# Performance work log

Measured on AMD Instinct MI355X. Metric: run time of the kernel, lower is better.

Reference implementation:

```python
import jax, jax.numpy as jnp
import numpy as np

B, N, D = 8, 2048, 256      # batch, tokens, model dim (= out_token_dims)
S = 128                     # query_key_dims
H = int(2.0 * D)            # expansion_factor * D = 512
EPS = 1e-5


def setup_inputs() -> dict:
    key = jax.random.key(0)
    ks = jax.random.split(key, 4)
    x = jax.random.normal(ks[0], (B, N, D), dtype=jnp.float32)
    g = jnp.ones((), jnp.float32)                                # ScaleNorm gain
    W_uv = jax.random.normal(ks[1], (D, 2 * H + S), jnp.float32) * 0.02
    b_uv = jnp.zeros((2 * H + S,), jnp.float32)
    gamma = jnp.ones((2, S), jnp.float32)                        # OffsetScale scale
    beta = jnp.zeros((2, S), jnp.float32)                        # OffsetScale offset
    W_o = jax.random.normal(ks[2], (H, D), jnp.float32) * 0.02
    b_o = jnp.zeros((D,), jnp.float32)
    return {"x": x, "g": g, "W_uv": W_uv, "b_uv": b_uv,
            "gamma": gamma, "beta": beta, "W_o": W_o, "b_o": b_o}


def reference(x, g, W_uv, b_uv, gamma, beta, W_o, b_o):
    d = x.shape[-1]
    # ScaleNorm: x / max(||x|| / sqrt(d), eps) * g
    norm = jnp.linalg.norm(x, axis=-1, keepdims=True) * jax.lax.rsqrt(jnp.float32(d))
    xn = x / jnp.maximum(norm, EPS) * g
    # fused uv projection + SiLU
    uv = jax.nn.silu(jnp.einsum('bnd,de->bne', xn, W_uv) + b_uv)
    u = uv[..., :H]            # gate branch        [B,N,H]
    v = uv[..., H:2 * H]       # value branch       [B,N,H]
    base = uv[..., 2 * H:]     # shared q/k base    [B,N,S]
    # OffsetScale heads=2 -> q, k (cheap per-dim affine)
    q = base * gamma[0] + beta[0]
    k = base * gamma[1] + beta[1]
    # single-head scores + ReLU^2 attention activation
    qk = jnp.einsum('bns,bms->bnm', q, k) * jax.lax.rsqrt(jnp.float32(S))
    attn = jnp.square(jax.nn.relu(qk))
    # gate * (attn @ v), then output projection back to D
    gated = u * jnp.einsum('bnm,bmh->bnh', attn, v)
    return jnp.einsum('bnh,hd->bnd', gated, W_o) + b_o
```

## Files before the change

kernel.cpp:

```cpp
#include <hip/hip_runtime.h>
#include <math.h>

#define BB 8
#define NN 2048
#define DD 256
#define SS 128
#define HH 512
#define EE 1152

typedef short bf16x8 __attribute__((ext_vector_type(8)));
typedef float f32x4 __attribute__((ext_vector_type(4)));

__device__ __forceinline__ short f2bf(float f) {
    union { float f; unsigned u; } a; a.f = f;
    unsigned r = a.u + 0x7FFFu + ((a.u >> 16) & 1u);
    return (short)(r >> 16);
}
__device__ __forceinline__ float bf2f(short s) {
    union { unsigned u; float f; } a; a.u = ((unsigned)(unsigned short)s) << 16;
    return a.f;
}
__device__ __forceinline__ void gl_lds16(const short* g, short* l) {
    __builtin_amdgcn_global_load_lds(
        (const __attribute__((address_space(1))) void*)g,
        (__attribute__((address_space(3))) void*)l, 16, 0, 0);
}

__global__ __launch_bounds__(256) void k_pre(
        const float* __restrict__ x, const float* __restrict__ gp,
        short* __restrict__ xn,
        const float* __restrict__ Wuv, const float* __restrict__ Wo,
        short* __restrict__ Wuv_t, short* __restrict__ Wo_t) {
    __shared__ float tile[32][33];
    int bid = blockIdx.x;
    int t = threadIdx.x;
    if (bid < 4096) {
        int wave = t >> 6, lane = t & 63;
        long row = (long)bid * 4 + wave;
        float4 xv = ((const float4*)(x + row * DD))[lane];
        float ss = xv.x*xv.x + xv.y*xv.y + xv.z*xv.z + xv.w*xv.w;
        #pragma unroll
        for (int off = 32; off > 0; off >>= 1) ss += __shfl_down(ss, off);
        ss = __shfl(ss, 0);
        float norm = sqrtf(ss) * 0.0625f;
        float scale = gp[0] / fmaxf(norm, 1e-5f);
        short4 o;
        o.x = f2bf(xv.x * scale); o.y = f2bf(xv.y * scale);
        o.z = f2bf(xv.z * scale); o.w = f2bf(xv.w * scale);
        ((short4*)(xn + row * DD))[lane] = o;
    } else if (bid < 4384) {
        int bid2 = bid - 4096;
        int et = bid2 % 36, dt = bid2 / 36;
        #pragma unroll
        for (int i = 0; i < 4; i++) {
            int idx = t + i*256, r = idx >> 5, c = idx & 31;
            tile[r][c] = Wuv[(long)(dt*32 + r)*EE + et*32 + c];
        }
        __syncthreads();
        #pragma unroll
        for (int i = 0; i < 4; i++) {
            int idx = t + i*256, r = idx >> 5, c = idx & 31;
            Wuv_t[(long)(et*32 + r)*DD + dt*32 + c] = f2bf(tile[c][r]);
        }
    } else {
        int bid3 = bid - 4384;
        int ht = bid3 % 16, dt = bid3 / 16;
        #pragma unroll
        for (int i = 0; i < 4; i++) {
            int idx = t + i*256, r = idx >> 5, c = idx & 31;
            tile[r][c] = Wo[(long)(ht*32 + r)*DD + dt*32 + c];
        }
        __syncthreads();
        #pragma unroll
        for (int i = 0; i < 4; i++) {
            int idx = t + i*256, r = idx >> 5, c = idx & 31;
            Wo_t[(long)(dt*32 + r)*HH + ht*32 + c] = f2bf(tile[c][r]);
        }
    }
}

__global__ __launch_bounds__(256) void k_gemm1(
        const short* __restrict__ xn, const short* __restrict__ Wuv_t,
        const float* __restrict__ b_uv,
        const float* __restrict__ gamma, const float* __restrict__ beta,
        short* __restrict__ u, short* __restrict__ vfrag,
        short* __restrict__ q, short* __restrict__ k) {
    __shared__ short As[128*64];
    __shared__ short Bs[128*64];
    int m0 = blockIdx.x * 128, n0 = blockIdx.y * 128;
    int t = threadIdx.x, w = t >> 6, lane = t & 63;
    int wr = w & 1, wc = w >> 1, l16 = lane & 15, quad = lane >> 4;
    int lr = lane >> 3, lc = (lane & 7) * 8;
    f32x4 acc[4][4] = {};
    for (int k0 = 0; k0 < DD; k0 += 64) {
        __syncthreads();
        #pragma unroll
        for (int i = 0; i < 4; i++) {
            int r0 = i*32 + w*8;
            gl_lds16(&xn[(long)(m0 + r0 + lr)*DD + k0 + lc], &As[r0*64]);
            gl_lds16(&Wuv_t[(long)(n0 + r0 + lr)*DD + k0 + lc], &Bs[r0*64]);
        }
        __syncthreads();
        #pragma unroll
        for (int kk = 0; kk < 2; kk++) {
            bf16x8 a[4], bb[4];
            #pragma unroll
            for (int mt = 0; mt < 4; mt++)
                a[mt] = *(const bf16x8*)&As[(wr*64 + mt*16 + l16)*64 + kk*32 + quad*8];
            #pragma unroll
            for (int nt = 0; nt < 4; nt++)
                bb[nt] = *(const bf16x8*)&Bs[(wc*64 + nt*16 + l16)*64 + kk*32 + quad*8];
            #pragma unroll
            for (int mt = 0; mt < 4; mt++)
                #pragma unroll
                for (int nt = 0; nt < 4; nt++)
                    acc[mt][nt] = __builtin_amdgcn_mfma_f32_16x16x32_bf16(
                        a[mt], bb[nt], acc[mt][nt], 0,0,0);
        }
    }
    #pragma unroll
    for (int mt = 0; mt < 4; mt++)
    #pragma unroll
    for (int nt = 0; nt < 4; nt++) {
        int gm0 = m0 + wr*64 + mt*16 + quad*4;
        int ge  = n0 + wc*64 + nt*16 + l16;
        float val[4];
        #pragma unroll
        for (int r = 0; r < 4; r++) {
            float xv = acc[mt][nt][r] + b_uv[ge];
            val[r] = xv / (1.0f + __expf(-xv));
        }
        if (ge < HH) {
            #pragma unroll
            for (int r = 0; r < 4; r++)
                u[(long)(gm0 + r)*HH + ge] = f2bf(val[r]);
        } else if (ge < 2*HH) {
            int h = ge - HH;
            long base = (((long)((gm0 >> 11)*64 + ((gm0 & 2047) >> 5)) * 32)
                         + (h >> 4)) * 512
                        + ((((gm0 & 31) >> 3)*16 + (h & 15)) * 8) + (gm0 & 7);
            short4 o;
            o.x = f2bf(val[0]); o.y = f2bf(val[1]);
            o.z = f2bf(val[2]); o.w = f2bf(val[3]);
            *(short4*)&vfrag[base] = o;
        } else {
            int si = ge - 2*HH;
            #pragma unroll
            for (int r = 0; r < 4; r++) {
                q[(long)(gm0 + r)*SS + si] = f2bf(val[r] * gamma[si]      + beta[si]);
                k[(long)(gm0 + r)*SS + si] = f2bf(val[r] * gamma[SS + si] + beta[SS + si]);
            }
        }
    }
}

#define KS(p,row)  (smem + ((p)*32 + (row))*136)
#define PS(p,row)  (smem + 8704 + ((p)*64 + (row))*40)
#define GT(hf,row) (smem + (hf)*16896 + (row)*264)

__global__ __launch_bounds__(512, 2) void k_attn(
        const short* __restrict__ q, const short* __restrict__ k,
        const short* __restrict__ vfrag, const short* __restrict__ u,
        const short* __restrict__ Wo_t, const float* __restrict__ b_o,
        float* __restrict__ out) {
    extern __shared__ __align__(16) short smem[];
    int b = blockIdx.x & 7;
    int i0 = (blockIdx.x >> 3) * 64;
    int t = threadIdx.x, w = t >> 6, lane = t & 63;
    int l16 = lane & 15, quad = lane >> 4;
    int qt = w >> 1, mt = w & 1;
    const short* qb  = q + ((long)b * NN + i0) * SS;
    const short* kb  = k + (long)b * NN * SS;
    const short* vfb = vfrag + (long)b * 64 * 32 * 512;
    const float RS = 0.08838834764831845f;

    int krow = t >> 4, kch = (t & 15) * 8;

    bf16x8 qf[4];
    #pragma unroll
    for (int kc = 0; kc < 4; kc++)
        qf[kc] = *(const bf16x8*)&qb[(long)(qt*16 + l16)*SS + kc*32 + quad*8];

    *(bf16x8*)&KS(0,krow)[kch] = *(const bf16x8*)&kb[(long)krow*SS + kch];
    bf16x8 kpre = *(const bf16x8*)&kb[(long)(32 + krow)*SS + kch];
    __syncthreads();

    f32x4 acc[16] = {};
    for (int it = 0; it < NN/32; it++) {
        int p = it & 1;
        int m0 = it * 32;
        int mnext = (m0 + 64 < NN) ? m0 + 64 : m0;
        bf16x8 knext = *(const bf16x8*)&kb[(long)(mnext + krow)*SS + kch];
        bf16x8 vf[4];
        #pragma unroll
        for (int jj = 0; jj < 4; jj++)
            vf[jj] = *(const bf16x8*)&vfb[((long)it*32 + (w*4 + jj))*512 + lane*8];
        f32x4 sc = {};
        #pragma unroll
        for (int kc = 0; kc < 4; kc++) {
            bf16x8 kf = *(const bf16x8*)&KS(p, mt*16 + l16)[kc*32 + quad*8];
            sc = __builtin_amdgcn_mfma_f32_16x16x32_bf16(kf, qf[kc], sc, 0,0,0);
        }
        short4 pw;
        {
            float s0 = fmaxf(sc[0]*RS, 0.f), s1 = fmaxf(sc[1]*RS, 0.f);
            float s2 = fmaxf(sc[2]*RS, 0.f), s3 = fmaxf(sc[3]*RS, 0.f);
            pw.x = f2bf(s0*s0); pw.y = f2bf(s1*s1);
            pw.z = f2bf(s2*s2); pw.w = f2bf(s3*s3);
        }
        *(short4*)&PS(p, qt*16 + l16)[mt*16 + quad*4] = pw;
        *(bf16x8*)&KS(p^1, krow)[kch] = kpre;
        kpre = knext;
        __syncthreads();
        bf16x8 af[4];
        #pragma unroll
        for (int qq2 = 0; qq2 < 4; qq2++)
            af[qq2] = *(const bf16x8*)&PS(p, qq2*16 + l16)[quad*8];
        #pragma unroll
        for (int jj = 0; jj < 4; jj++)
            #pragma unroll
            for (int qq2 = 0; qq2 < 4; qq2++)
                acc[qq2*4 + jj] = __builtin_amdgcn_mfma_f32_16x16x32_bf16(
                    af[qq2], vf[jj], acc[qq2*4 + jj], 0,0,0);
    }

    long rowbase = (long)b * NN + i0;
    __syncthreads();
    {
        int hf = w >> 2;
        int hbase = (w & 3) * 64;
        #pragma unroll
        for (int qq2 = 0; qq2 < 4; qq2++)
        #pragma unroll
        for (int jj = 0; jj < 4; jj++) {
            int gh = w*64 + jj*16 + l16;
            #pragma unroll
            for (int r = 0; r < 4; r++) {
                long grow = rowbase + qq2*16 + quad*4 + r;
                float uval = bf2f(u[grow*HH + gh]);
                GT(hf, qq2*16 + quad*4 + r)[hbase + jj*16 + l16] =
                    f2bf(acc[qq2*4 + jj][r] * uval);
            }
        }
    }
    __syncthreads();
    f32x4 acc2[4][2] = {};
    #pragma unroll
    for (int p = 0; p < 2; p++) {
        #pragma unroll
        for (int kc = 0; kc < 8; kc++) {
            bf16x8 A[4], Bf[2];
            #pragma unroll
            for (int mt2 = 0; mt2 < 4; mt2++)
                A[mt2] = *(const bf16x8*)&GT(p, mt2*16 + l16)[kc*32 + quad*8];
            #pragma unroll
            for (int nt = 0; nt < 2; nt++)
                Bf[nt] = *(const bf16x8*)&Wo_t[(long)(w*32 + nt*16 + l16)*HH
                                               + p*256 + kc*32 + quad*8];
            #pragma unroll
            for (int mt2 = 0; mt2 < 4; mt2++)
                #pragma unroll
                for (int nt = 0; nt < 2; nt++)
                    acc2[mt2][nt] = __builtin_amdgcn_mfma_f32_16x16x32_bf16(
                        A[mt2], Bf[nt], acc2[mt2][nt], 0,0,0);
        }
    }
    #pragma unroll
    for (int mt2 = 0; mt2 < 4; mt2++)
    #pragma unroll
    for (int nt = 0; nt < 2; nt++)
    #pragma unroll
    for (int r = 0; r < 4; r++) {
        long grow = rowbase + mt2*16 + quad*4 + r;
        int gd = w*32 + nt*16 + l16;
        out[grow*DD + gd] = acc2[mt2][nt][r] + b_o[gd];
    }
}

extern "C" void kernel_launch(void* const* d_in, const int* in_sizes, int n_in,
                              void* d_out, int out_size, void* d_ws, size_t ws_size,
                              hipStream_t stream) {
    const float* x     = (const float*)d_in[0];
    const float* g     = (const float*)d_in[1];
    const float* Wuv   = (const float*)d_in[2];
    const float* b_uv  = (const float*)d_in[3];
    const float* gamma = (const float*)d_in[4];
    const float* beta  = (const float*)d_in[5];
    const float* Wo    = (const float*)d_in[6];
    const float* b_o   = (const float*)d_in[7];
    float* out = (float*)d_out;

    short* ws    = (short*)d_ws;
    short* xn    = ws;
    short* Wuv_t = xn    + (long)16384 * 256;
    short* Wo_t  = Wuv_t + (long)1152 * 256;
    short* u     = Wo_t  + (long)256 * 512;
    short* vfrag = u     + (long)16384 * 512;
    short* qq    = vfrag + (long)16384 * 512;
    short* kk    = qq    + (long)16384 * 128;

    k_pre<<<4512, 256, 0, stream>>>(x, g, xn, Wuv, Wo, Wuv_t, Wo_t);
    k_gemm1<<<dim3(128, 9), 256, 0, stream>>>(xn, Wuv_t, b_uv, gamma, beta,
                                              u, vfrag, qq, kk);
    k_attn<<<256, 512, 67584, stream>>>(qq, kk, vfrag, u, Wo_t, b_o, out);
}
```

Baseline: 169.1 us.

## Double-buffer gemm1 k-loop and restructure attention kernel to 1024 threads with swizzled LDS

The first GEMM now uses a 32-wide K step with double-buffered LDS, prefetching the next tile while computing on the current one, which removes one barrier per step. The attention kernel moves to 1024 threads (16 waves), processes 64 keys per iteration, and switches K, P and gated-tile LDS layouts to XOR-swizzled addressing to avoid bank conflicts. It also raises MFMA wave priority around the P·V product and splits the output projection across 16 waves. The larger block and launch bounds of four waves per SIMD cap register use per thread, which risks spills, and LDS drops slightly to 64KB.

```diff
diff --git a/kernel.cpp b/kernel.cpp
--- a/kernel.cpp
+++ b/kernel.cpp
@@ -85,38 +85,45 @@
         const float* __restrict__ gamma, const float* __restrict__ beta,
         short* __restrict__ u, short* __restrict__ vfrag,
         short* __restrict__ q, short* __restrict__ k) {
-    __shared__ short As[128*64];
-    __shared__ short Bs[128*64];
+    __shared__ short As[2][128*32];
+    __shared__ short Bs[2][128*32];
     int m0 = blockIdx.x * 128, n0 = blockIdx.y * 128;
     int t = threadIdx.x, w = t >> 6, lane = t & 63;
     int wr = w & 1, wc = w >> 1, l16 = lane & 15, quad = lane >> 4;
-    int lr = lane >> 3, lc = (lane & 7) * 8;
+    int lr = lane >> 2, lc = (lane & 3) * 8;
     f32x4 acc[4][4] = {};
-    for (int k0 = 0; k0 < DD; k0 += 64) {
+    #pragma unroll
+    for (int i = 0; i < 2; i++) {
+        int r0 = i*64 + w*16;
+        gl_lds16(&xn[(long)(m0 + r0 + lr)*DD + lc], &As[0][r0*32]);
+        gl_lds16(&Wuv_t[(long)(n0 + r0 + lr)*DD + lc], &Bs[0][r0*32]);
+    }
+    __syncthreads();
+    for (int ks = 0; ks < 8; ks++) {
+        int cur = ks & 1;
+        if (ks < 7) {
+            int k0 = (ks + 1) * 32, nb = cur ^ 1;
+            #pragma unroll
+            for (int i = 0; i < 2; i++) {
+                int r0 = i*64 + w*16;
+                gl_lds16(&xn[(long)(m0 + r0 + lr)*DD + k0 + lc], &As[nb][r0*32]);
+                gl_lds16(&Wuv_t[(long)(n0 + r0 + lr)*DD + k0 + lc], &Bs[nb][r0*32]);
+            }
+        }
+        bf16x8 a[4], bb[4];
+        #pragma unroll
+        for (int mt = 0; mt < 4; mt++)
+            a[mt] = *(const bf16x8*)&As[cur][(wr*64 + mt*16 + l16)*32 + quad*8];
+        #pragma unroll
+        for (int nt = 0; nt < 4; nt++)
+            bb[nt] = *(const bf16x8*)&Bs[cur][(wc*64 + nt*16 + l16)*32 + quad*8];
+        #pragma unroll
+        for (int mt = 0; mt < 4; mt++)
+            #pragma unroll
+            for (int nt = 0; nt < 4; nt++)
+                acc[mt][nt] = __builtin_amdgcn_mfma_f32_16x16x32_bf16(
+                    a[mt], bb[nt], acc[mt][nt], 0,0,0);
         __syncthreads();
-        #pragma unroll
-        for (int i = 0; i < 4; i++) {
-            int r0 = i*32 + w*8;
-            gl_lds16(&xn[(long)(m0 + r0 + lr)*DD + k0 + lc], &As[r0*64]);
-            gl_lds16(&Wuv_t[(long)(n0 + r0 + lr)*DD + k0 + lc], &Bs[r0*64]);
-        }
-        __syncthreads();
-        #pragma unroll
-        for (int kk = 0; kk < 2; kk++) {
-            bf16x8 a[4], bb[4];
-            #pragma unroll
-            for (int mt = 0; mt < 4; mt++)
-                a[mt] = *(const bf16x8*)&As[(wr*64 + mt*16 + l16)*64 + kk*32 + quad*8];
-            #pragma unroll
-            for (int nt = 0; nt < 4; nt++)
-                bb[nt] = *(const bf16x8*)&Bs[(wc*64 + nt*16 + l16)*64 + kk*32 + quad*8];
-            #pragma unroll
-            for (int mt = 0; mt < 4; mt++)
-                #pragma unroll
-                for (int nt = 0; nt < 4; nt++)
-                    acc[mt][nt] = __builtin_amdgcn_mfma_f32_16x16x32_bf16(
-                        a[mt], bb[nt], acc[mt][nt], 0,0,0);
-        }
     }
     #pragma unroll
     for (int mt = 0; mt < 4; mt++)
@@ -154,11 +161,11 @@
     }
 }
 
-#define KS(p,row)  (smem + ((p)*32 + (row))*136)
-#define PS(p,row)  (smem + 8704 + ((p)*64 + (row))*40)
-#define GT(hf,row) (smem + (hf)*16896 + (row)*264)
-
-__global__ __launch_bounds__(512, 2) void k_attn(
+#define KSW(pp,row,cb) (smem + ((pp)*64 + (row))*128 + (((cb) ^ (((row)&3)<<6)) >> 1))
+#define PSW(pp,row,cb) (smem + 16384 + ((pp)*64 + (row))*64 + (((cb) ^ (((row)&3)<<5)) >> 1))
+#define GTW(row,cb)    (smem + (row)*512 + (((cb) ^ (((row)&7)<<6)) >> 1))
+
+__global__ __launch_bounds__(1024, 4) void k_attn(
         const short* __restrict__ q, const short* __restrict__ k,
         const short* __restrict__ vfrag, const short* __restrict__ u,
         const short* __restrict__ Wo_t, const float* __restrict__ b_o,
@@ -168,37 +175,40 @@
     int i0 = (blockIdx.x >> 3) * 64;
     int t = threadIdx.x, w = t >> 6, lane = t & 63;
     int l16 = lane & 15, quad = lane >> 4;
-    int qt = w >> 1, mt = w & 1;
+    int qt = w >> 2, mtile = w & 3;
     const short* qb  = q + ((long)b * NN + i0) * SS;
     const short* kb  = k + (long)b * NN * SS;
     const short* vfb = vfrag + (long)b * 64 * 32 * 512;
     const float RS = 0.08838834764831845f;
 
-    int krow = t >> 4, kch = (t & 15) * 8;
+    int krow = t >> 4, kch = t & 15;
 
     bf16x8 qf[4];
     #pragma unroll
     for (int kc = 0; kc < 4; kc++)
         qf[kc] = *(const bf16x8*)&qb[(long)(qt*16 + l16)*SS + kc*32 + quad*8];
 
-    *(bf16x8*)&KS(0,krow)[kch] = *(const bf16x8*)&kb[(long)krow*SS + kch];
-    bf16x8 kpre = *(const bf16x8*)&kb[(long)(32 + krow)*SS + kch];
+    *(bf16x8*)KSW(0, krow, kch*16) = *(const bf16x8*)&kb[(long)krow*SS + kch*8];
+    bf16x8 kpre = *(const bf16x8*)&kb[(long)(64 + krow)*SS + kch*8];
     __syncthreads();
 
-    f32x4 acc[16] = {};
-    for (int it = 0; it < NN/32; it++) {
+    f32x4 acc[4][2] = {};
+    for (int it = 0; it < NN/64; it++) {
         int p = it & 1;
-        int m0 = it * 32;
-        int mnext = (m0 + 64 < NN) ? m0 + 64 : m0;
-        bf16x8 knext = *(const bf16x8*)&kb[(long)(mnext + krow)*SS + kch];
-        bf16x8 vf[4];
-        #pragma unroll
-        for (int jj = 0; jj < 4; jj++)
-            vf[jj] = *(const bf16x8*)&vfb[((long)it*32 + (w*4 + jj))*512 + lane*8];
+        int m0 = it * 64;
+        int mnext = (m0 + 128 < NN) ? m0 + 128 : m0;
+        bf16x8 knext = *(const bf16x8*)&kb[(long)(mnext + krow)*SS + kch*8];
+        bf16x8 vf[2][2];
+        #pragma unroll
+        for (int s = 0; s < 2; s++)
+            #pragma unroll
+            for (int j = 0; j < 2; j++)
+                vf[s][j] = *(const bf16x8*)
+                    &vfb[((long)(it*2 + s)*32 + (w*2 + j))*512 + lane*8];
         f32x4 sc = {};
         #pragma unroll
         for (int kc = 0; kc < 4; kc++) {
-            bf16x8 kf = *(const bf16x8*)&KS(p, mt*16 + l16)[kc*32 + quad*8];
+            bf16x8 kf = *(const bf16x8*)KSW(p, mtile*16 + l16, kc*64 + quad*16);
             sc = __builtin_amdgcn_mfma_f32_16x16x32_bf16(kf, qf[kc], sc, 0,0,0);
         }
         short4 pw;
@@ -208,72 +218,61 @@
             pw.x = f2bf(s0*s0); pw.y = f2bf(s1*s1);
             pw.z = f2bf(s2*s2); pw.w = f2bf(s3*s3);
         }
-        *(short4*)&PS(p, qt*16 + l16)[mt*16 + quad*4] = pw;
-        *(bf16x8*)&KS(p^1, krow)[kch] = kpre;
+        *(short4*)PSW(p, qt*16 + l16, mtile*32 + quad*8) = pw;
+        *(bf16x8*)KSW(p^1, krow, kch*16) = kpre;
         kpre = knext;
         __syncthreads();
-        bf16x8 af[4];
-        #pragma unroll
-        for (int qq2 = 0; qq2 < 4; qq2++)
-            af[qq2] = *(const bf16x8*)&PS(p, qq2*16 + l16)[quad*8];
-        #pragma unroll
-        for (int jj = 0; jj < 4; jj++)
-            #pragma unroll
-            for (int qq2 = 0; qq2 < 4; qq2++)
-                acc[qq2*4 + jj] = __builtin_amdgcn_mfma_f32_16x16x32_bf16(
-                    af[qq2], vf[jj], acc[qq2*4 + jj], 0,0,0);
+        __builtin_amdgcn_s_setprio(1);
+        #pragma unroll
+        for (int s = 0; s < 2; s++) {
+            bf16x8 af[4];
+            #pragma unroll
+            for (int qq = 0; qq < 4; qq++)
+                af[qq] = *(const bf16x8*)PSW(p, qq*16 + l16, s*64 + quad*16);
+            #pragma unroll
+            for (int qq = 0; qq < 4; qq++)
+                #pragma unroll
+                for (int j = 0; j < 2; j++)
+                    acc[qq][j] = __builtin_amdgcn_mfma_f32_16x16x32_bf16(
+                        af[qq], vf[s][j], acc[qq][j], 0,0,0);
+        }
+        __builtin_amdgcn_s_setprio(0);
     }
 
     long rowbase = (long)b * NN + i0;
     __syncthreads();
-    {
-        int hf = w >> 2;
-        int hbase = (w & 3) * 64;
-        #pragma unroll
-        for (int qq2 = 0; qq2 < 4; qq2++)
-        #pragma unroll
-        for (int jj = 0; jj < 4; jj++) {
-            int gh = w*64 + jj*16 + l16;
-            #pragma unroll
-            for (int r = 0; r < 4; r++) {
-                long grow = rowbase + qq2*16 + quad*4 + r;
-                float uval = bf2f(u[grow*HH + gh]);
-                GT(hf, qq2*16 + quad*4 + r)[hbase + jj*16 + l16] =
-                    f2bf(acc[qq2*4 + jj][r] * uval);
-            }
+    #pragma unroll
+    for (int qq = 0; qq < 4; qq++)
+    #pragma unroll
+    for (int j = 0; j < 2; j++) {
+        int gh = w*32 + j*16 + l16;
+        #pragma unroll
+        for (int r = 0; r < 4; r++) {
+            int row = qq*16 + quad*4 + r;
+            float uval = bf2f(u[(rowbase + row)*HH + gh]);
+            *GTW(row, 2*gh) = f2bf(acc[qq][j][r] * uval);
         }
     }
     __syncthreads();
-    f32x4 acc2[4][2] = {};
-    #pragma unroll
-    for (int p = 0; p < 2; p++) {
-        #pragma unroll
-        for (int kc = 0; kc < 8; kc++) {
-            bf16x8 A[4], Bf[2];
-            #pragma unroll
-            for (int mt2 = 0; mt2 < 4; mt2++)
-                A[mt2] = *(const bf16x8*)&GT(p, mt2*16 + l16)[kc*32 + quad*8];
-            #pragma unroll
-            for (int nt = 0; nt < 2; nt++)
-                Bf[nt] = *(const bf16x8*)&Wo_t[(long)(w*32 + nt*16 + l16)*HH
-                                               + p*256 + kc*32 + quad*8];
-            #pragma unroll
-            for (int mt2 = 0; mt2 < 4; mt2++)
-                #pragma unroll
-                for (int nt = 0; nt < 2; nt++)
-                    acc2[mt2][nt] = __builtin_amdgcn_mfma_f32_16x16x32_bf16(
-                        A[mt2], Bf[nt], acc2[mt2][nt], 0,0,0);
-        }
-    }
-    #pragma unroll
-    for (int mt2 = 0; mt2 < 4; mt2++)
-    #pragma unroll
-    for (int nt = 0; nt < 2; nt++)
+    f32x4 acc2[4] = {};
+    #pragma unroll
+    for (int kc = 0; kc < 16; kc++) {
+        bf16x8 A[4];
+        #pragma unroll
+        for (int qq = 0; qq < 4; qq++)
+            A[qq] = *(const bf16x8*)GTW(qq*16 + l16, kc*64 + quad*16);
+        bf16x8 Bf = *(const bf16x8*)&Wo_t[(long)(w*16 + l16)*HH + kc*32 + quad*8];
+        #pragma unroll
+        for (int qq = 0; qq < 4; qq++)
+            acc2[qq] = __builtin_amdgcn_mfma_f32_16x16x32_bf16(A[qq], Bf, acc2[qq], 0,0,0);
+    }
+    #pragma unroll
+    for (int qq = 0; qq < 4; qq++)
     #pragma unroll
     for (int r = 0; r < 4; r++) {
-        long grow = rowbase + mt2*16 + quad*4 + r;
-        int gd = w*32 + nt*16 + l16;
-        out[grow*DD + gd] = acc2[mt2][nt][r] + b_o[gd];
+        long grow = rowbase + qq*16 + quad*4 + r;
+        int gd = w*16 + l16;
+        out[grow*DD + gd] = acc2[qq][r] + b_o[gd];
     }
 }
 
@@ -302,5 +301,5 @@
     k_pre<<<4512, 256, 0, stream>>>(x, g, xn, Wuv, Wo, Wuv_t, Wo_t);
     k_gemm1<<<dim3(128, 9), 256, 0, stream>>>(xn, Wuv_t, b_uv, gamma, beta,
                                               u, vfrag, qq, kk);
-    k_attn<<<256, 512, 67584, stream>>>(qq, kk, vfrag, u, Wo_t, b_o, out);
-}
+    k_attn<<<256, 1024, 65536, stream>>>(qq, kk, vfrag, u, Wo_t, b_o, out);
+}
```

Result: no change. 166.8 us (-1.3%).
